# Kernel optimization log

Measured on AMD Instinct MI355X. Metric: run time of the kernel, lower is better.

The kernel has to match this reference:

```python
import jax, jax.numpy as jnp
import numpy as np

N, F_IN, HID, E = 100000, 128, 64, 3200000


def setup_inputs() -> dict:
    key = jax.random.key(0)
    ks = jax.random.split(key, 12)
    s = 0.05
    inp = {
        "x": jax.random.normal(ks[0], (N, F_IN), jnp.float32),
        "edge_index": jax.random.randint(ks[1], (2, E), 0, N, dtype=jnp.int32),
        "edge_weight": jax.random.uniform(ks[2], (E,), jnp.float32),
    }
    C = F_IN + HID  # DConv input channels = cat([X, H])
    # DConv weights have shape (2, K, in_channels, out_channels); K = 1 here.
    inp["Wz"] = s * jax.random.normal(ks[3], (2, 1, C, HID), jnp.float32)
    inp["bz"] = jnp.zeros((HID,), jnp.float32)
    inp["Wr"] = s * jax.random.normal(ks[4], (2, 1, C, HID), jnp.float32)
    inp["br"] = jnp.zeros((HID,), jnp.float32)
    inp["Wh"] = s * jax.random.normal(ks[5], (2, 1, C, HID), jnp.float32)
    inp["bh"] = jnp.zeros((HID,), jnp.float32)
    inp["Wlin"] = s * jax.random.normal(ks[6], (HID, 1), jnp.float32)
    inp["blin"] = jnp.zeros((1,), jnp.float32)
    return inp


def _dconv_k1(Y, W, b):
    # DConv with K=1: only the 0-th Chebyshev term of both diffusion
    # directions is used -> Y @ (W[0,0] + W[1,0]) + b. No propagation.
    return jnp.matmul(Y, W[0, 0] + W[1, 0]) + b


def reference(x, edge_index, edge_weight, Wz, bz, Wr, br, Wh, bh, Wlin, blin):
    n = x.shape[0]
    # Faithful-but-unused: original DConv normalizes edge weights by
    # out/in degree before the K>1 check; with K=1 it never affects output.
    row, col = edge_index[0], edge_index[1]
    deg_out = jax.ops.segment_sum(edge_weight, row, num_segments=n)
    deg_in = jax.ops.segment_sum(edge_weight, col, num_segments=n)
    _norm_out = jnp.where(deg_out[row] > 0, edge_weight / deg_out[row], 0.0)
    _norm_in = jnp.where(deg_in[col] > 0, edge_weight / deg_in[col], 0.0)

    H0 = jnp.zeros((n, Wz.shape[-1]), x.dtype)  # _set_hidden_state -> zeros
    XH = jnp.concatenate([x, H0], axis=1)       # [N, F_IN + HID]
    Z = jax.nn.sigmoid(_dconv_k1(XH, Wz, bz))   # update gate
    R = jax.nn.sigmoid(_dconv_k1(XH, Wr, br))   # reset gate
    XRH = jnp.concatenate([x, R * H0], axis=1)
    H_tilde = jnp.tanh(_dconv_k1(XRH, Wh, bh))
    H = Z * H0 + (1.0 - Z) * H_tilde            # GRU state update

    h = jax.nn.relu(H)
    # dropout: identity in eval mode (deterministic reference)
    return jnp.matmul(h, Wlin) + blin            # [N, 1]
```

## Files before the change

### kernel.cpp

```cpp
#include <hip/hip_runtime.h>
#include <hip/hip_bf16.h>

using bf16x8 = __attribute__((ext_vector_type(8))) short;
using f32x4  = __attribute__((ext_vector_type(4))) float;

static constexpr int kN          = 100000;
static constexpr int kFIN        = 128;
static constexpr int kTermStride = 192 * 64;
static constexpr int kTiles      = kN / 16;
static constexpr int kBlocks     = 768;
static constexpr int kWaves      = kBlocks * 4;
static constexpr int kBaseTiles  = kWaves * 2;
static constexpr int kExtra      = kTiles - kBaseTiles;

__device__ __forceinline__ short f2bf(float v) {
    union { float f; unsigned u; } a; a.f = v;
    unsigned r = a.u + 0x7fffu + ((a.u >> 16) & 1u);
    return (short)(r >> 16);
}

__device__ __forceinline__ float rcp_fast(float x) { return __builtin_amdgcn_rcpf(x); }
__device__ __forceinline__ float sigmoid_fast(float x) {
    return rcp_fast(1.0f + __expf(-x));
}
__device__ __forceinline__ float tanh_fast(float x) {
    float e = __expf(2.0f * x);
    return 1.0f - 2.0f * rcp_fast(e + 1.0f);
}

__global__ __launch_bounds__(256, 4) void fused_gcn(
    const float* __restrict__ x,
    const float* __restrict__ Wz,
    const float* __restrict__ bz,
    const float* __restrict__ Wh,
    const float* __restrict__ bh,
    const float* __restrict__ wlin,
    const float* __restrict__ blin,
    float* __restrict__ out)
{
    __shared__ short lw[16384];

    const int t    = threadIdx.x;
    const int wid  = t >> 6;
    const int lane = t & 63;
    const int r    = lane & 15;
    const int g    = lane >> 4;
    const int gw   = blockIdx.x * 4 + wid;
    const int t0   = gw * 2, t1 = t0 + 1;
    const int t2   = (gw < kExtra) ? kBaseTiles + gw : -1;

    f32x4 f[8];
    auto load_x = [&](int tile) {
        const float* xrow = x + (size_t)(tile * 16 + r) * kFIN;
        #pragma unroll
        for (int kk = 0; kk < 4; ++kk) {
            f[kk * 2]     = *(const f32x4*)(xrow + kk * 32 + g * 8);
            f[kk * 2 + 1] = *(const f32x4*)(xrow + kk * 32 + g * 8 + 4);
        }
    };

    load_x(t0);

    #pragma unroll
    for (int mat = 0; mat < 2; ++mat) {
        const float* W = mat ? Wh : Wz;
        #pragma unroll
        for (int it = 0; it < 8; ++it) {
            int fidx = it * 1024 + t * 4;
            f32x4 w0 = *(const f32x4*)(W + fidx);
            f32x4 w1 = *(const f32x4*)(W + kTermStride + fidx);
            #pragma unroll
            for (int i = 0; i < 4; ++i) {
                int fi = fidx + i;
                int k = fi >> 6, c = fi & 63;
                int kk = k >> 5, gg = (k >> 3) & 3, e = k & 7;
                int jt = c >> 4, ln = gg * 16 + (c & 15);
                lw[((mat * 4 + kk) * 4 + jt) * 512 + ln * 8 + e] = f2bf(w0[i] + w1[i]);
            }
        }
    }
    __syncthreads();

    float bzc[4], bhc[4], wlc[4];
    #pragma unroll
    for (int jt = 0; jt < 4; ++jt) {
        int c = jt * 16 + r;
        bzc[jt] = bz[c]; bhc[jt] = bh[c]; wlc[jt] = wlin[c];
    }
    const float bl = blin[0];

    bf16x8 a[4];
    auto cvt = [&]() {
        #pragma unroll
        for (int kk = 0; kk < 4; ++kk) {
            #pragma unroll
            for (int e = 0; e < 4; ++e) {
                a[kk][e]     = f2bf(f[kk * 2][e]);
                a[kk][e + 4] = f2bf(f[kk * 2 + 1][e]);
            }
        }
    };

    auto compute_tile = [&](int tile) {
        f32x4 accz[4], acch[4];
        #pragma unroll
        for (int jt = 0; jt < 4; ++jt) {
            accz[jt] = f32x4{0.f, 0.f, 0.f, 0.f};
            acch[jt] = f32x4{0.f, 0.f, 0.f, 0.f};
        }
        #pragma unroll
        for (int kk = 0; kk < 4; ++kk) {
            #pragma unroll
            for (int jt = 0; jt < 4; ++jt) {
                bf16x8 wz = *(const bf16x8*)&lw[((0 * 4 + kk) * 4 + jt) * 512 + lane * 8];
                bf16x8 wh = *(const bf16x8*)&lw[((1 * 4 + kk) * 4 + jt) * 512 + lane * 8];
                accz[jt] = __builtin_amdgcn_mfma_f32_16x16x32_bf16(a[kk], wz, accz[jt], 0, 0, 0);
                acch[jt] = __builtin_amdgcn_mfma_f32_16x16x32_bf16(a[kk], wh, acch[jt], 0, 0, 0);
            }
        }
        float contrib[4] = {0.f, 0.f, 0.f, 0.f};
        #pragma unroll
        for (int jt = 0; jt < 4; ++jt) {
            #pragma unroll
            for (int i = 0; i < 4; ++i) {
                float z  = sigmoid_fast(accz[jt][i] + bzc[jt]);
                float ht = tanh_fast(acch[jt][i] + bhc[jt]);
                float H  = (1.0f - z) * ht;
                contrib[i] += (H > 0.f ? H : 0.f) * wlc[jt];
            }
        }
        #pragma unroll
        for (int m = 1; m < 16; m <<= 1) {
            #pragma unroll
            for (int i = 0; i < 4; ++i)
                contrib[i] += __shfl_xor(contrib[i], m, 64);
        }
        if (r == 0) {
            #pragma unroll
            for (int i = 0; i < 4; ++i)
                out[tile * 16 + g * 4 + i] = contrib[i] + bl;
        }
    };

    cvt();
    load_x(t1);
    compute_tile(t0);
    cvt();
    if (t2 >= 0) load_x(t2);
    compute_tile(t1);
    if (t2 >= 0) {
        cvt();
        compute_tile(t2);
    }
}

extern "C" void kernel_launch(void* const* d_in, const int* in_sizes, int n_in,
                              void* d_out, int out_size, void* d_ws, size_t ws_size,
                              hipStream_t stream) {
    const float* x    = (const float*)d_in[0];
    const float* Wz   = (const float*)d_in[3];
    const float* bz   = (const float*)d_in[4];
    const float* Wh   = (const float*)d_in[7];
    const float* bh   = (const float*)d_in[8];
    const float* wlin = (const float*)d_in[9];
    const float* blin = (const float*)d_in[10];

    fused_gcn<<<dim3(kBlocks), dim3(256), 0, stream>>>(
        x, Wz, bz, Wh, bh, wlin, blin, (float*)d_out);
}
```

Measured before the change: 19.44 us.

## Use 1024 blocks with strided two-tile work and precomputed LDS weight addressing

Raises the grid from 768 to 1024 blocks, so each wave handles at most two tiles (gw and gw+kWaves) instead of two or three. The per-element LDS index calculation for the weight prep is replaced by one precomputed byte base per thread plus constant offsets. The epilogue uses fmaxf and a single vector store for the four outputs. The aim is to even out the tail, cut integer work in the prologue, and shorten the store path, at the cost of more blocks each redoing the weight-staging prologue.

```diff
diff --git a/kernel.cpp b/kernel.cpp
--- a/kernel.cpp
+++ b/kernel.cpp
@@ -8,10 +8,8 @@
 static constexpr int kFIN        = 128;
 static constexpr int kTermStride = 192 * 64;
 static constexpr int kTiles      = kN / 16;
-static constexpr int kBlocks     = 768;
+static constexpr int kBlocks     = 1024;
 static constexpr int kWaves      = kBlocks * 4;
-static constexpr int kBaseTiles  = kWaves * 2;
-static constexpr int kExtra      = kTiles - kBaseTiles;
 
 __device__ __forceinline__ short f2bf(float v) {
     union { float f; unsigned u; } a; a.f = v;
@@ -46,8 +44,8 @@
     const int r    = lane & 15;
     const int g    = lane >> 4;
     const int gw   = blockIdx.x * 4 + wid;
-    const int t0   = gw * 2, t1 = t0 + 1;
-    const int t2   = (gw < kExtra) ? kBaseTiles + gw : -1;
+    const int t0   = gw;
+    const int t1   = (gw + kWaves < kTiles) ? gw + kWaves : -1;
 
     f32x4 f[8];
     auto load_x = [&](int tile) {
@@ -61,26 +59,6 @@
 
     load_x(t0);
 
-    #pragma unroll
-    for (int mat = 0; mat < 2; ++mat) {
-        const float* W = mat ? Wh : Wz;
-        #pragma unroll
-        for (int it = 0; it < 8; ++it) {
-            int fidx = it * 1024 + t * 4;
-            f32x4 w0 = *(const f32x4*)(W + fidx);
-            f32x4 w1 = *(const f32x4*)(W + kTermStride + fidx);
-            #pragma unroll
-            for (int i = 0; i < 4; ++i) {
-                int fi = fidx + i;
-                int k = fi >> 6, c = fi & 63;
-                int kk = k >> 5, gg = (k >> 3) & 3, e = k & 7;
-                int jt = c >> 4, ln = gg * 16 + (c & 15);
-                lw[((mat * 4 + kk) * 4 + jt) * 512 + ln * 8 + e] = f2bf(w0[i] + w1[i]);
-            }
-        }
-    }
-    __syncthreads();
-
     float bzc[4], bhc[4], wlc[4];
     #pragma unroll
     for (int jt = 0; jt < 4; ++jt) {
@@ -88,6 +66,28 @@
         bzc[jt] = bz[c]; bhc[jt] = bh[c]; wlc[jt] = wlin[c];
     }
     const float bl = blin[0];
+
+    {
+        const int s  = t >> 4;
+        const int c0 = (t << 2) & 63;
+        char* dstb = (char*)lw +
+            ((c0 >> 4) * 512 + (s >> 3) * 128 + (c0 & 15) * 8 + (s & 7)) * 2;
+        #pragma unroll
+        for (int mat = 0; mat < 2; ++mat) {
+            const float* W = mat ? Wh : Wz;
+            #pragma unroll
+            for (int it = 0; it < 8; ++it) {
+                const int fidx = it * 1024 + t * 4;
+                f32x4 w0 = *(const f32x4*)(W + fidx);
+                f32x4 w1 = *(const f32x4*)(W + kTermStride + fidx);
+                const int off = (mat * 8192 + (it >> 1) * 2048 + (it & 1) * 256) * 2;
+                #pragma unroll
+                for (int i = 0; i < 4; ++i)
+                    *(short*)(dstb + off + i * 16) = f2bf(w0[i] + w1[i]);
+            }
+        }
+    }
+    __syncthreads();
 
     bf16x8 a[4];
     auto cvt = [&]() {
@@ -112,8 +112,8 @@
         for (int kk = 0; kk < 4; ++kk) {
             #pragma unroll
             for (int jt = 0; jt < 4; ++jt) {
-                bf16x8 wz = *(const bf16x8*)&lw[((0 * 4 + kk) * 4 + jt) * 512 + lane * 8];
-                bf16x8 wh = *(const bf16x8*)&lw[((1 * 4 + kk) * 4 + jt) * 512 + lane * 8];
+                bf16x8 wz = *(const bf16x8*)&lw[(kk * 4 + jt) * 512 + lane * 8];
+                bf16x8 wh = *(const bf16x8*)&lw[8192 + (kk * 4 + jt) * 512 + lane * 8];
                 accz[jt] = __builtin_amdgcn_mfma_f32_16x16x32_bf16(a[kk], wz, accz[jt], 0, 0, 0);
                 acch[jt] = __builtin_amdgcn_mfma_f32_16x16x32_bf16(a[kk], wh, acch[jt], 0, 0, 0);
             }
@@ -126,7 +126,7 @@
                 float z  = sigmoid_fast(accz[jt][i] + bzc[jt]);
                 float ht = tanh_fast(acch[jt][i] + bhc[jt]);
                 float H  = (1.0f - z) * ht;
-                contrib[i] += (H > 0.f ? H : 0.f) * wlc[jt];
+                contrib[i] += fmaxf(H, 0.f) * wlc[jt];
             }
         }
         #pragma unroll
@@ -136,21 +136,19 @@
                 contrib[i] += __shfl_xor(contrib[i], m, 64);
         }
         if (r == 0) {
+            f32x4 o;
             #pragma unroll
-            for (int i = 0; i < 4; ++i)
-                out[tile * 16 + g * 4 + i] = contrib[i] + bl;
+            for (int i = 0; i < 4; ++i) o[i] = contrib[i] + bl;
+            *(f32x4*)(out + tile * 16 + g * 4) = o;
         }
     };
 
     cvt();
-    load_x(t1);
+    if (t1 >= 0) load_x(t1);
     compute_tile(t0);
-    cvt();
-    if (t2 >= 0) load_x(t2);
-    compute_tile(t1);
-    if (t2 >= 0) {
+    if (t1 >= 0) {
         cvt();
-        compute_tile(t2);
+        compute_tile(t1);
     }
 }
 
```

New measurement: 21.07 us. 8.4% more time.

## Pre-pack combined bf16 weights in a separate kernel and copy into LDS

Applied to the files above, without the earlier changes.

Adds a small prep kernel that sums the two diffusion weight terms, converts them to bf16 and writes them once to workspace in the MFMA fragment layout. The main kernel then does a straight int4 copy into LDS instead of every block loading fp32 weights, converting and scattering them. Output stores become one vector store per group, and the launch bounds occupancy hint drops from 4 to 3. This trades a second kernel launch and a dependency between the two kernels for less per-block prologue work.

```diff
diff --git a/kernel.cpp b/kernel.cpp
--- a/kernel.cpp
+++ b/kernel.cpp
@@ -6,7 +6,7 @@
 
 static constexpr int kN          = 100000;
 static constexpr int kFIN        = 128;
-static constexpr int kTermStride = 192 * 64;
+static constexpr int kC          = 192;
 static constexpr int kTiles      = kN / 16;
 static constexpr int kBlocks     = 768;
 static constexpr int kWaves      = kBlocks * 4;
@@ -28,11 +28,26 @@
     return 1.0f - 2.0f * rcp_fast(e + 1.0f);
 }
 
-__global__ __launch_bounds__(256, 4) void fused_gcn(
+__global__ void prep_weights(const float* __restrict__ Wz,
+                             const float* __restrict__ Wh,
+                             short* __restrict__ wpack) {
+    int idx = blockIdx.x * blockDim.x + threadIdx.x;
+    if (idx >= 2 * kFIN * 64) return;
+    int mat = idx >> 13;
+    int rem = idx & 8191;
+    int k = rem >> 6;
+    int c = rem & 63;
+    const float* W = mat ? Wh : Wz;
+    float v = W[k * 64 + c] + W[kC * 64 + k * 64 + c];
+    int kk = k >> 5, g = (k >> 3) & 3, e = k & 7;
+    int jt = c >> 4, ln = g * 16 + (c & 15);
+    wpack[((mat * 4 + kk) * 4 + jt) * 512 + ln * 8 + e] = f2bf(v);
+}
+
+__global__ __launch_bounds__(256, 3) void fused_gcn(
     const float* __restrict__ x,
-    const float* __restrict__ Wz,
+    const short* __restrict__ wpack,
     const float* __restrict__ bz,
-    const float* __restrict__ Wh,
     const float* __restrict__ bh,
     const float* __restrict__ wlin,
     const float* __restrict__ blin,
@@ -61,26 +76,6 @@
 
     load_x(t0);
 
-    #pragma unroll
-    for (int mat = 0; mat < 2; ++mat) {
-        const float* W = mat ? Wh : Wz;
-        #pragma unroll
-        for (int it = 0; it < 8; ++it) {
-            int fidx = it * 1024 + t * 4;
-            f32x4 w0 = *(const f32x4*)(W + fidx);
-            f32x4 w1 = *(const f32x4*)(W + kTermStride + fidx);
-            #pragma unroll
-            for (int i = 0; i < 4; ++i) {
-                int fi = fidx + i;
-                int k = fi >> 6, c = fi & 63;
-                int kk = k >> 5, gg = (k >> 3) & 3, e = k & 7;
-                int jt = c >> 4, ln = gg * 16 + (c & 15);
-                lw[((mat * 4 + kk) * 4 + jt) * 512 + ln * 8 + e] = f2bf(w0[i] + w1[i]);
-            }
-        }
-    }
-    __syncthreads();
-
     float bzc[4], bhc[4], wlc[4];
     #pragma unroll
     for (int jt = 0; jt < 4; ++jt) {
@@ -88,6 +83,14 @@
         bzc[jt] = bz[c]; bhc[jt] = bh[c]; wlc[jt] = wlin[c];
     }
     const float bl = blin[0];
+
+    {
+        const int4* src = (const int4*)wpack;
+        int4* dst = (int4*)lw;
+        #pragma unroll
+        for (int i = 0; i < 8; ++i) dst[t + 256 * i] = src[t + 256 * i];
+    }
+    __syncthreads();
 
     bf16x8 a[4];
     auto cvt = [&]() {
@@ -112,8 +115,8 @@
         for (int kk = 0; kk < 4; ++kk) {
             #pragma unroll
             for (int jt = 0; jt < 4; ++jt) {
-                bf16x8 wz = *(const bf16x8*)&lw[((0 * 4 + kk) * 4 + jt) * 512 + lane * 8];
-                bf16x8 wh = *(const bf16x8*)&lw[((1 * 4 + kk) * 4 + jt) * 512 + lane * 8];
+                bf16x8 wz = *(const bf16x8*)&lw[(kk * 4 + jt) * 512 + lane * 8];
+                bf16x8 wh = *(const bf16x8*)&lw[8192 + (kk * 4 + jt) * 512 + lane * 8];
                 accz[jt] = __builtin_amdgcn_mfma_f32_16x16x32_bf16(a[kk], wz, accz[jt], 0, 0, 0);
                 acch[jt] = __builtin_amdgcn_mfma_f32_16x16x32_bf16(a[kk], wh, acch[jt], 0, 0, 0);
             }
@@ -126,7 +129,7 @@
                 float z  = sigmoid_fast(accz[jt][i] + bzc[jt]);
                 float ht = tanh_fast(acch[jt][i] + bhc[jt]);
                 float H  = (1.0f - z) * ht;
-                contrib[i] += (H > 0.f ? H : 0.f) * wlc[jt];
+                contrib[i] += fmaxf(H, 0.f) * wlc[jt];
             }
         }
         #pragma unroll
@@ -136,9 +139,10 @@
                 contrib[i] += __shfl_xor(contrib[i], m, 64);
         }
         if (r == 0) {
+            f32x4 o;
             #pragma unroll
-            for (int i = 0; i < 4; ++i)
-                out[tile * 16 + g * 4 + i] = contrib[i] + bl;
+            for (int i = 0; i < 4; ++i) o[i] = contrib[i] + bl;
+            *(f32x4*)(out + tile * 16 + g * 4) = o;
         }
     };
 
@@ -164,7 +168,9 @@
     const float* bh   = (const float*)d_in[8];
     const float* wlin = (const float*)d_in[9];
     const float* blin = (const float*)d_in[10];
+    short* wpack = (short*)d_ws;
 
+    prep_weights<<<dim3(64), dim3(256), 0, stream>>>(Wz, Wh, wpack);
     fused_gcn<<<dim3(kBlocks), dim3(256), 0, stream>>>(
-        x, Wz, bz, Wh, bh, wlin, blin, (float*)d_out);
+        x, wpack, bz, bh, wlin, blin, (float*)d_out);
 }
```

Result: slower. 22.95 us (+18.1%).
